# Kernel tuning notes

Hardware: AMD Instinct MI355X
Metric: run time of the kernel (lower is better)

Reference implementation:

```python
import jax, jax.numpy as jnp
import numpy as np

N_REL = 16   # n_relation
EMB = 512    # emb_size
N = 32768    # number of nodes/tokens


def setup_inputs() -> dict:
    key = jax.random.key(0)
    k1, k2, k3 = jax.random.split(key, 3)
    node_emb = jax.random.normal(k1, (N, EMB), dtype=jnp.float32)
    relation = jax.random.randint(k2, (N,), 0, N_REL)
    # nn.Linear default init: U(-1/sqrt(in_features), 1/sqrt(in_features))
    bound = 1.0 / np.sqrt(EMB)
    W = jax.random.uniform(k3, (N_REL, EMB, EMB), dtype=jnp.float32,
                           minval=-bound, maxval=bound)
    return {"node_emb": node_emb, "relation": relation, "W": W}


def reference(node_emb, relation, W):
    # out[i] = W[relation[i]] @ node_emb[i]  (F.linear(x, W_r) == x @ W_r.T)
    # Loop over the small fixed relation set via lax.scan; tokens stay vectorized.
    n_rel = W.shape[0]
    out0 = jnp.zeros((node_emb.shape[0], W.shape[1]), dtype=node_emb.dtype)

    def body(acc, wr):
        Wr, r = wr
        y = node_emb @ Wr.T                       # [N, EMB]
        acc = jnp.where((relation == r)[:, None], y, acc)
        return acc, None

    out, _ = jax.lax.scan(body, out0, (W, jnp.arange(n_rel)))
    return out
```

## Files before the change

### kernel.cpp

```cpp
#include <hip/hip_runtime.h>
#include <stdint.h>


#define EMB 512
#define N_RELC 16
#define BM 128
#define BN 128
#define BK 32
#define NKT 16

typedef __attribute__((ext_vector_type(4))) float f32x4;
typedef __attribute__((ext_vector_type(8))) short bf16x8;

__device__ __forceinline__ unsigned short f2bf(float f) {
  unsigned int u = __float_as_uint(f);
  u += 0x7FFFu + ((u >> 16) & 1u);
  return (unsigned short)(u >> 16);
}

__device__ __forceinline__ bf16x8 cvt8(f32x4 lo, f32x4 hi) {
  bf16x8 o;
  o[0] = (short)f2bf(lo[0]); o[1] = (short)f2bf(lo[1]);
  o[2] = (short)f2bf(lo[2]); o[3] = (short)f2bf(lo[3]);
  o[4] = (short)f2bf(hi[0]); o[5] = (short)f2bf(hi[1]);
  o[6] = (short)f2bf(hi[2]); o[7] = (short)f2bf(hi[3]);
  return o;
}

__device__ __forceinline__ void gload_lds16(const void* g, void* l) {
  __builtin_amdgcn_global_load_lds(
      (const __attribute__((address_space(1))) unsigned int*)(uintptr_t)g,
      (__attribute__((address_space(3))) unsigned int*)(uintptr_t)l, 16, 0, 0);
}

__global__ __launch_bounds__(256) void histo_rank_fill(
    const int* __restrict__ rel, int* cnt, int* pos, int* ptok,
    int n, int padn) {
  __shared__ int lcnt[N_RELC];
  __shared__ int lbase[N_RELC];
  const int tid = threadIdx.x;
  if (tid < N_RELC) lcnt[tid] = 0;
  __syncthreads();
  const int i = blockIdx.x * blockDim.x + tid;
  if (i < padn) ptok[i] = -1;
  int r = 0, myrank = 0;
  if (i < n) { r = rel[i]; myrank = atomicAdd(&lcnt[r], 1); }
  __syncthreads();
  if (tid < N_RELC) lbase[tid] = atomicAdd(&cnt[tid], lcnt[tid]);
  __syncthreads();
  if (i < n) pos[i] = lbase[r] + myrank;
}

__global__ void prefix_tiles64(const int* __restrict__ cnt, int* pbase,
                               int* tinfo, int maxt) {
  __shared__ int sb[N_RELC + 1];
  __shared__ int st[N_RELC + 1];
  if (threadIdx.x == 0) {
    int acc = 0, t = 0;
    for (int r = 0; r < N_RELC; ++r) {
      sb[r] = acc; st[r] = t;
      const int nt = (cnt[r] + BM - 1) / BM;
      acc += nt * BM;
      t += nt;
    }
    sb[N_RELC] = acc; st[N_RELC] = t;
  }
  __syncthreads();
  for (int i = threadIdx.x; i <= N_RELC; i += blockDim.x) pbase[i] = sb[i];
  for (int x = threadIdx.x; x < maxt; x += blockDim.x) {
    int v = -1;
    #pragma unroll
    for (int r = 0; r < N_RELC; ++r)
      if (x >= st[r] && x < st[r + 1]) v = (r << 16) | (x - st[r]);
    tinfo[x] = v;
  }
}

__global__ __launch_bounds__(256) void scatter_ptok(
    const int* __restrict__ rel, const int* __restrict__ pos,
    const int* __restrict__ pbase, int* __restrict__ ptok, int n) {
  const int i = blockIdx.x * blockDim.x + threadIdx.x;
  if (i < n) ptok[pbase[rel[i]] + pos[i]] = i;
}

__global__ __launch_bounds__(256) void convert_W(const float* __restrict__ W,
                                                 unsigned short* __restrict__ Ws,
                                                 int welems) {
  const size_t i = ((size_t)blockIdx.x * 256 + threadIdx.x) * 8;
  if (i >= (size_t)welems) return;
  f32x4 a = *reinterpret_cast<const f32x4*>(W + i);
  f32x4 c = *reinterpret_cast<const f32x4*>(W + i + 4);
  bf16x8 o;
  o[0] = f2bf(a[0]); o[1] = f2bf(a[1]); o[2] = f2bf(a[2]); o[3] = f2bf(a[3]);
  o[4] = f2bf(c[0]); o[5] = f2bf(c[1]); o[6] = f2bf(c[2]); o[7] = f2bf(c[3]);
  *reinterpret_cast<bf16x8*>(Ws + i) = o;
}


#define STAGE(S, KT)                                                           \
  {                                                                            \
    const int kb_ = (KT) * BK;                                                 \
    gload_lds16(asrc0 + kb_, (char*)&As[S][0] + tid * 16);                     \
    gload_lds16(asrc1 + kb_, (char*)&As[S][0] + 4096 + tid * 16);              \
    gload_lds16(asrc2 + kb_, (char*)&As[S][0] + 8192 + tid * 16);              \
    gload_lds16(asrc3 + kb_, (char*)&As[S][0] + 12288 + tid * 16);             \
    gload_lds16(bsrc0 + kb_, (char*)&Bs[S][0] + tid * 16);                     \
    gload_lds16(bsrc1 + kb_, (char*)&Bs[S][0] + 4096 + tid * 16);              \
  }

#define COMPUTE(S)                                                             \
  {                                                                            \
    bf16x8 af[4], bfr[4];                                                      \
    _Pragma("unroll")                                                          \
    for (int m = 0; m < 4; ++m) {                                              \
      const int rr_ = wr * 64 + m * 16 + lrow;                                 \
      const char* base_ = (const char*)&As[S][0] + rr_ * 128;                  \
      f32x4 lo = *reinterpret_cast<const f32x4*>(                              \
          base_ + (((gl * 2) ^ (rr_ & 7)) * 16));                              \
      f32x4 hi = *reinterpret_cast<const f32x4*>(                              \
          base_ + (((gl * 2 + 1) ^ (rr_ & 7)) * 16));                          \
      af[m] = cvt8(lo, hi);                                                    \
    }                                                                          \
    _Pragma("unroll")                                                          \
    for (int nn = 0; nn < 4; ++nn) {                                           \
      const int rw_ = wc * 64 + nn * 16 + lrow;                                \
      bfr[nn] = *reinterpret_cast<const bf16x8*>(                              \
          (const char*)&Bs[S][0] + rw_ * 64 + ((gl ^ ((rw_ >> 1) & 3)) * 16)); \
    }                                                                          \
    _Pragma("unroll")                                                          \
    for (int m = 0; m < 4; ++m)                                                \
      _Pragma("unroll")                                                        \
      for (int nn = 0; nn < 4; ++nn)                                           \
        acc[m][nn] = __builtin_amdgcn_mfma_f32_16x16x32_bf16(                  \
            af[m], bfr[nn], acc[m][nn], 0, 0, 0);                              \
  }

#define ITER(T, VM)                                                            \
  {                                                                            \
    if ((T) + 2 < NKT) STAGE(((T) + 2) % 3, (T) + 2);                          \
    asm volatile("s_waitcnt vmcnt(" #VM ")" ::: "memory");                     \
    __builtin_amdgcn_s_barrier();                                              \
    __builtin_amdgcn_sched_barrier(0);                                         \
    COMPUTE((T) % 3);                                                          \
    asm volatile("s_waitcnt lgkmcnt(0)" ::: "memory");                         \
    __builtin_amdgcn_s_barrier();                                              \
    __builtin_amdgcn_sched_barrier(0);                                         \
  }

__global__ __launch_bounds__(256, 2) void gg11(
    const float* __restrict__ X, const unsigned short* __restrict__ Ws,
    const int* __restrict__ pbase, const int* __restrict__ tinfo,
    const int* __restrict__ ptok, float* __restrict__ out)
{
  __shared__ float As[3][BM * BK];
  __shared__ unsigned short Bs[3][BN * BK];

  const int q = gridDim.x >> 3;
  const int lid = ((int)blockIdx.x & 7) * q + ((int)blockIdx.x >> 3);
  const int info = tinfo[lid >> 2];
  if (info < 0) return;
  const int r = info >> 16;
  const int mt = info & 0xFFFF;
  const int ct = lid & 3;
  const int prow0 = pbase[r] + mt * BM;

  const int tid = threadIdx.x;
  const int lane = tid & 63;
  const int wid = tid >> 6;
  const int wr = wid >> 1, wc = wid & 1;
  const int lrow = lane & 15;
  const int gl = lane >> 4;

  const int arow = tid >> 3;
  const int aslot = (tid & 7) ^ (arow & 7);
  int t0 = ptok[prow0 + arow];        if (t0 < 0) t0 = 0;
  int t1 = ptok[prow0 + 32 + arow];   if (t1 < 0) t1 = 0;
  int t2 = ptok[prow0 + 64 + arow];   if (t2 < 0) t2 = 0;
  int t3 = ptok[prow0 + 96 + arow];   if (t3 < 0) t3 = 0;
  const float* asrc0 = X + (size_t)t0 * EMB + aslot * 4;
  const float* asrc1 = X + (size_t)t1 * EMB + aslot * 4;
  const float* asrc2 = X + (size_t)t2 * EMB + aslot * 4;
  const float* asrc3 = X + (size_t)t3 * EMB + aslot * 4;
  const int brow = tid >> 2;
  const int bgran = (tid & 3) ^ ((tid >> 3) & 3);
  const unsigned short* bsrc0 =
      Ws + ((size_t)r * EMB + (size_t)(ct * BN + brow)) * EMB + bgran * 8;
  const unsigned short* bsrc1 = bsrc0 + (size_t)64 * EMB;

  f32x4 acc[4][4];
  const f32x4 vzero = {0.f, 0.f, 0.f, 0.f};
  #pragma unroll
  for (int m = 0; m < 4; ++m)
    #pragma unroll
    for (int nn = 0; nn < 4; ++nn) acc[m][nn] = vzero;

  STAGE(0, 0);
  STAGE(1, 1);

  ITER(0, 12)  ITER(1, 12)  ITER(2, 12)  ITER(3, 12)
  ITER(4, 12)  ITER(5, 12)  ITER(6, 12)  ITER(7, 12)
  ITER(8, 12)  ITER(9, 12)  ITER(10, 12) ITER(11, 12)
  ITER(12, 12) ITER(13, 12) ITER(14, 6)  ITER(15, 0)

  #pragma unroll
  for (int m = 0; m < 4; ++m) {
    const int base = prow0 + wr * 64 + m * 16 + gl * 4;
    #pragma unroll
    for (int rg = 0; rg < 4; ++rg) {
      const int tok = ptok[base + rg];
      if (tok >= 0) {
        float* orow = out + (size_t)tok * EMB + ct * BN + wc * 64;
        #pragma unroll
        for (int nn = 0; nn < 4; ++nn)
          orow[nn * 16 + lrow] = acc[m][nn][rg];
      }
    }
  }
}

__global__ void naive_kernel(const float* __restrict__ X, const int* __restrict__ rel,
                             const float* __restrict__ W, float* __restrict__ out, int n) {
  int i = blockIdx.x;
  if (i >= n) return;
  int r = rel[i];
  const float* x = X + (size_t)i * EMB;
  const float* Wr = W + (size_t)r * EMB * EMB;
  for (int j = threadIdx.x; j < EMB; j += blockDim.x) {
    const float* w = Wr + (size_t)j * EMB;
    float s = 0.f;
    for (int k = 0; k < EMB; ++k) s += w[k] * x[k];
    out[(size_t)i * EMB + j] = s;
  }
}

extern "C" void kernel_launch(void* const* d_in, const int* in_sizes, int n_in,
                              void* d_out, int out_size, void* d_ws, size_t ws_size,
                              hipStream_t stream) {
  const float* X  = (const float*)d_in[0];
  const int* rel  = (const int*)d_in[1];
  const float* W  = (const float*)d_in[2];
  float* out      = (float*)d_out;
  const int n = in_sizes[1];
  const int welems = in_sizes[2];
  const int padn = n + N_RELC * BM;
  const int maxt = (n + BM - 1) / BM + N_RELC;
  const int maxtp = ((maxt + 1) / 2) * 2;

  const size_t ints = (size_t)64 + n + padn + maxtp;
  const size_t offW = ((ints * sizeof(int) + 255) / 256) * 256;
  const size_t need = offW + (size_t)welems * 2;

  if (ws_size < need) {
    naive_kernel<<<n, 256, 0, stream>>>(X, rel, W, out, n);
    return;
  }

  int* cnt   = (int*)d_ws;
  int* pbase = cnt + 16;
  int* pos   = cnt + 64;
  int* ptok  = pos + n;
  int* tinfo = ptok + padn;
  unsigned short* Ws = (unsigned short*)((char*)d_ws + offW);

  hipMemsetAsync(cnt, 0, 64 * sizeof(int), stream);
  histo_rank_fill<<<(padn + 255) / 256, 256, 0, stream>>>(rel, cnt, pos, ptok, n, padn);
  prefix_tiles64<<<1, 64, 0, stream>>>(cnt, pbase, tinfo, maxtp);
  scatter_ptok<<<(n + 255) / 256, 256, 0, stream>>>(rel, pos, pbase, ptok, n);
  convert_W<<<(welems / 8 + 255) / 256, 256, 0, stream>>>(W, Ws, welems);

  gg11<<<4 * maxtp, 256, 0, stream>>>(X, Ws, pbase, tinfo, ptok, out);
}
```

Measured before the change: 71.58 us.

## Widen grouped GEMM tile to 256 columns and stage A via registers as bf16

Doubles the output-column tile to 256 with 512-thread blocks, so each gathered token row is loaded from global memory half as often. The fp32 A tile is now loaded into registers, converted to bf16 once and written to LDS, rather than being copied to LDS as fp32 and converted on every read. This halves A's LDS footprint and removes per-wave conversion work. It also adds setprio around the MFMA block and replaces the memset with a tiny init kernel, at the cost of more register pressure and a deeper software pipeline.

```diff
diff --git a/kernel.cpp b/kernel.cpp
--- a/kernel.cpp
+++ b/kernel.cpp
@@ -5,7 +5,7 @@
 #define EMB 512
 #define N_RELC 16
 #define BM 128
-#define BN 128
+#define BN 256
 #define BK 32
 #define NKT 16
 
@@ -31,6 +31,10 @@
   __builtin_amdgcn_global_load_lds(
       (const __attribute__((address_space(1))) unsigned int*)(uintptr_t)g,
       (__attribute__((address_space(3))) unsigned int*)(uintptr_t)l, 16, 0, 0);
+}
+
+__global__ void init_counts(int* cnt) {
+  if (threadIdx.x < 32) cnt[threadIdx.x] = 0;
 }
 
 __global__ __launch_bounds__(256) void histo_rank_fill(
@@ -97,15 +101,24 @@
 }
 
 
-#define STAGE(S, KT)                                                           \
+#define ALOAD(P, KT)                                                           \
+  {                                                                            \
+    const float* ap_ = aptr + (KT) * BK;                                       \
+    a##P##0 = *reinterpret_cast<const f32x4*>(ap_);                            \
+    a##P##1 = *reinterpret_cast<const f32x4*>(ap_ + 4);                        \
+  }
+
+#define AWRITE(S, P)                                                           \
+  {                                                                            \
+    bf16x8 w_ = cvt8(a##P##0, a##P##1);                                        \
+    *reinterpret_cast<bf16x8*>((char*)&As[S][0] + awoff) = w_;                 \
+  }
+
+#define BSTAGE(S, KT)                                                          \
   {                                                                            \
     const int kb_ = (KT) * BK;                                                 \
-    gload_lds16(asrc0 + kb_, (char*)&As[S][0] + tid * 16);                     \
-    gload_lds16(asrc1 + kb_, (char*)&As[S][0] + 4096 + tid * 16);              \
-    gload_lds16(asrc2 + kb_, (char*)&As[S][0] + 8192 + tid * 16);              \
-    gload_lds16(asrc3 + kb_, (char*)&As[S][0] + 12288 + tid * 16);             \
     gload_lds16(bsrc0 + kb_, (char*)&Bs[S][0] + tid * 16);                     \
-    gload_lds16(bsrc1 + kb_, (char*)&Bs[S][0] + 4096 + tid * 16);              \
+    gload_lds16(bsrc1 + kb_, (char*)&Bs[S][0] + 8192 + tid * 16);              \
   }
 
 #define COMPUTE(S)                                                             \
@@ -114,12 +127,8 @@
     _Pragma("unroll")                                                          \
     for (int m = 0; m < 4; ++m) {                                              \
       const int rr_ = wr * 64 + m * 16 + lrow;                                 \
-      const char* base_ = (const char*)&As[S][0] + rr_ * 128;                  \
-      f32x4 lo = *reinterpret_cast<const f32x4*>(                              \
-          base_ + (((gl * 2) ^ (rr_ & 7)) * 16));                              \
-      f32x4 hi = *reinterpret_cast<const f32x4*>(                              \
-          base_ + (((gl * 2 + 1) ^ (rr_ & 7)) * 16));                          \
-      af[m] = cvt8(lo, hi);                                                    \
+      af[m] = *reinterpret_cast<const bf16x8*>(                                \
+          (const char*)&As[S][0] + rr_ * 64 + ((gl ^ ((rr_ >> 1) & 3)) * 16)); \
     }                                                                          \
     _Pragma("unroll")                                                          \
     for (int nn = 0; nn < 4; ++nn) {                                           \
@@ -127,65 +136,73 @@
       bfr[nn] = *reinterpret_cast<const bf16x8*>(                              \
           (const char*)&Bs[S][0] + rw_ * 64 + ((gl ^ ((rw_ >> 1) & 3)) * 16)); \
     }                                                                          \
+    __builtin_amdgcn_s_setprio(1);                                             \
     _Pragma("unroll")                                                          \
     for (int m = 0; m < 4; ++m)                                                \
       _Pragma("unroll")                                                        \
       for (int nn = 0; nn < 4; ++nn)                                           \
         acc[m][nn] = __builtin_amdgcn_mfma_f32_16x16x32_bf16(                  \
             af[m], bfr[nn], acc[m][nn], 0, 0, 0);                              \
+    __builtin_amdgcn_s_setprio(0);                                             \
   }
 
 #define ITER(T, VM)                                                            \
   {                                                                            \
-    if ((T) + 2 < NKT) STAGE(((T) + 2) % 3, (T) + 2);                          \
+    if ((T) + 2 < NKT) {                                                       \
+      if (((T) & 1) == 0) ALOAD(e, (T) + 2) else ALOAD(o, (T) + 2)             \
+      __builtin_amdgcn_sched_barrier(0);                                       \
+      BSTAGE(((T) + 2) % 3, (T) + 2);                                          \
+      __builtin_amdgcn_sched_barrier(0);                                       \
+    }                                                                          \
     asm volatile("s_waitcnt vmcnt(" #VM ")" ::: "memory");                     \
     __builtin_amdgcn_s_barrier();                                              \
     __builtin_amdgcn_sched_barrier(0);                                         \
+    if ((T) + 1 < NKT) {                                                       \
+      if ((((T) + 1) & 1) == 0) AWRITE(((T) + 1) % 3, e)                       \
+      else                      AWRITE(((T) + 1) % 3, o)                       \
+    }                                                                          \
     COMPUTE((T) % 3);                                                          \
     asm volatile("s_waitcnt lgkmcnt(0)" ::: "memory");                         \
     __builtin_amdgcn_s_barrier();                                              \
     __builtin_amdgcn_sched_barrier(0);                                         \
   }
 
-__global__ __launch_bounds__(256, 2) void gg11(
+__global__ __launch_bounds__(512, 4) void gg13(
     const float* __restrict__ X, const unsigned short* __restrict__ Ws,
     const int* __restrict__ pbase, const int* __restrict__ tinfo,
     const int* __restrict__ ptok, float* __restrict__ out)
 {
-  __shared__ float As[3][BM * BK];
+  __shared__ unsigned short As[3][BM * BK];
   __shared__ unsigned short Bs[3][BN * BK];
 
   const int q = gridDim.x >> 3;
   const int lid = ((int)blockIdx.x & 7) * q + ((int)blockIdx.x >> 3);
-  const int info = tinfo[lid >> 2];
+  const int info = tinfo[lid >> 1];
   if (info < 0) return;
   const int r = info >> 16;
   const int mt = info & 0xFFFF;
-  const int ct = lid & 3;
+  const int ct = lid & 1;
   const int prow0 = pbase[r] + mt * BM;
 
   const int tid = threadIdx.x;
   const int lane = tid & 63;
   const int wid = tid >> 6;
-  const int wr = wid >> 1, wc = wid & 1;
+  const int wr = wid >> 2;
+  const int wc = wid & 3;
   const int lrow = lane & 15;
   const int gl = lane >> 4;
 
-  const int arow = tid >> 3;
-  const int aslot = (tid & 7) ^ (arow & 7);
-  int t0 = ptok[prow0 + arow];        if (t0 < 0) t0 = 0;
-  int t1 = ptok[prow0 + 32 + arow];   if (t1 < 0) t1 = 0;
-  int t2 = ptok[prow0 + 64 + arow];   if (t2 < 0) t2 = 0;
-  int t3 = ptok[prow0 + 96 + arow];   if (t3 < 0) t3 = 0;
-  const float* asrc0 = X + (size_t)t0 * EMB + aslot * 4;
-  const float* asrc1 = X + (size_t)t1 * EMB + aslot * 4;
-  const float* asrc2 = X + (size_t)t2 * EMB + aslot * 4;
-  const float* asrc3 = X + (size_t)t3 * EMB + aslot * 4;
-  const int brow = tid >> 2;
-  const int bgran = (tid & 3) ^ ((tid >> 3) & 3);
+  const int srow = tid >> 2;
+  const int lg = tid & 3;
+  const int awoff = srow * 64 + ((lg ^ ((srow >> 1) & 3)) * 16);
+  int tokA = ptok[prow0 + srow];
+  if (tokA < 0) tokA = 0;
+  const float* aptr = X + (size_t)tokA * EMB + lg * 8;
+
+  const int blg = (tid & 3) ^ ((tid >> 3) & 3);
   const unsigned short* bsrc0 =
-      Ws + ((size_t)r * EMB + (size_t)(ct * BN + brow)) * EMB + bgran * 8;
-  const unsigned short* bsrc1 = bsrc0 + (size_t)64 * EMB;
+      Ws + ((size_t)r * EMB + (size_t)(ct * BN + srow)) * EMB + blg * 8;
+  const unsigned short* bsrc1 = bsrc0 + (size_t)128 * EMB;
 
   f32x4 acc[4][4];
   const f32x4 vzero = {0.f, 0.f, 0.f, 0.f};
@@ -194,13 +211,22 @@
     #pragma unroll
     for (int nn = 0; nn < 4; ++nn) acc[m][nn] = vzero;
 
-  STAGE(0, 0);
-  STAGE(1, 1);
-
-  ITER(0, 12)  ITER(1, 12)  ITER(2, 12)  ITER(3, 12)
-  ITER(4, 12)  ITER(5, 12)  ITER(6, 12)  ITER(7, 12)
-  ITER(8, 12)  ITER(9, 12)  ITER(10, 12) ITER(11, 12)
-  ITER(12, 12) ITER(13, 12) ITER(14, 6)  ITER(15, 0)
+  f32x4 ae0, ae1, ao0, ao1;
+
+  ALOAD(e, 0)
+  __builtin_amdgcn_sched_barrier(0);
+  BSTAGE(0, 0);
+  __builtin_amdgcn_sched_barrier(0);
+  ALOAD(o, 1)
+  __builtin_amdgcn_sched_barrier(0);
+  BSTAGE(1, 1);
+  __builtin_amdgcn_sched_barrier(0);
+  AWRITE(0, e)
+
+  ITER(0, 8)   ITER(1, 8)   ITER(2, 8)   ITER(3, 8)
+  ITER(4, 8)   ITER(5, 8)   ITER(6, 8)   ITER(7, 8)
+  ITER(8, 8)   ITER(9, 8)   ITER(10, 8)  ITER(11, 8)
+  ITER(12, 8)  ITER(13, 8)  ITER(14, 4)  ITER(15, 0)
 
   #pragma unroll
   for (int m = 0; m < 4; ++m) {
@@ -244,7 +270,7 @@
   const int welems = in_sizes[2];
   const int padn = n + N_RELC * BM;
   const int maxt = (n + BM - 1) / BM + N_RELC;
-  const int maxtp = ((maxt + 1) / 2) * 2;
+  const int maxtp = ((maxt + 3) / 4) * 4;
 
   const size_t ints = (size_t)64 + n + padn + maxtp;
   const size_t offW = ((ints * sizeof(int) + 255) / 256) * 256;
@@ -262,11 +288,11 @@
   int* tinfo = ptok + padn;
   unsigned short* Ws = (unsigned short*)((char*)d_ws + offW);
 
-  hipMemsetAsync(cnt, 0, 64 * sizeof(int), stream);
+  init_counts<<<1, 32, 0, stream>>>(cnt);
   histo_rank_fill<<<(padn + 255) / 256, 256, 0, stream>>>(rel, cnt, pos, ptok, n, padn);
   prefix_tiles64<<<1, 64, 0, stream>>>(cnt, pbase, tinfo, maxtp);
   scatter_ptok<<<(n + 255) / 256, 256, 0, stream>>>(rel, pos, pbase, ptok, n);
   convert_W<<<(welems / 8 + 255) / 256, 256, 0, stream>>>(W, Ws, welems);
 
-  gg11<<<4 * maxtp, 256, 0, stream>>>(X, Ws, pbase, tinfo, ptok, out);
-}
+  gg13<<<2 * maxtp, 512, 0, stream>>>(X, Ws, pbase, tinfo, ptok, out);
+}
```

After: 65.40 us. 1.09x faster.
